# Kernel tuning notes

Measured on AMD Instinct MI355X. Metric: run time of the kernel, lower is better.

Reference implementation:

```python
import jax, jax.numpy as jnp
import numpy as np

HIDDEN = 1024
HEADS = 16
HEAD_DIM = HIDDEN // HEADS


def setup_inputs() -> dict:
    key = jax.random.key(0)
    ks = jax.random.split(key, 7)
    B, S, H = 8, 1024, HIDDEN
    hidden_states = jax.random.normal(ks[0], (B, S, H), dtype=jnp.float32)
    attention_mask = jnp.zeros((B, 1, 1, S), dtype=jnp.float32)
    # Xavier-uniform weights [out, in], zero biases (matches module init)
    limit = float(np.sqrt(6.0 / (H + H)))
    Wq = jax.random.uniform(ks[1], (H, H), minval=-limit, maxval=limit, dtype=jnp.float32)
    Wk = jax.random.uniform(ks[2], (H, H), minval=-limit, maxval=limit, dtype=jnp.float32)
    Wv = jax.random.uniform(ks[3], (H, H), minval=-limit, maxval=limit, dtype=jnp.float32)
    bq = jnp.zeros((H,), dtype=jnp.float32)
    bk = jnp.zeros((H,), dtype=jnp.float32)
    bv = jnp.zeros((H,), dtype=jnp.float32)
    return {"hidden_states": hidden_states, "attention_mask": attention_mask,
            "Wq": Wq, "bq": bq, "Wk": Wk, "bk": bk, "Wv": Wv, "bv": bv}


def _split_heads(x):
    # [B, S, H] -> [B, heads, S, head_dim]
    B, S, _ = x.shape
    return x.reshape(B, S, HEADS, HEAD_DIM).transpose(0, 2, 1, 3)


def reference(hidden_states, attention_mask, Wq, bq, Wk, bk, Wv, bv):
    # Linear projections: y = x @ W^T + b  (weights stored [out, in] as in torch)
    q = _split_heads(hidden_states @ Wq.T + bq)
    k = _split_heads(hidden_states @ Wk.T + bk)
    v = _split_heads(hidden_states @ Wv.T + bv)
    scale = 1.0 / (HEAD_DIM ** 0.5)
    scores = jnp.einsum('bhqd,bhkd->bhqk', q, k) * scale  # [B,heads,S,S]
    scores = scores + attention_mask
    probs = jax.nn.softmax(scores, axis=-1)
    # dropout is identity at inference
    ctx = jnp.einsum('bhqk,bhkd->bhqd', probs, v)
    B, _, S, _ = ctx.shape
    return ctx.transpose(0, 2, 1, 3).reshape(B, S, HIDDEN)
```

## Files before the change

### kernel.cpp

```cpp
#include <hip/hip_runtime.h>
#include <hip/hip_bf16.h>
#include <stdint.h>

#define B_ 8
#define S_ 1024
#define NH_ 16
#define D_ 64
#define H_ 1024
#define M_TOT (B_*S_)
#define LOG2E 1.44269504088896f

typedef __attribute__((ext_vector_type(8))) short short8;
typedef __attribute__((ext_vector_type(4))) float f32x4;
typedef __attribute__((ext_vector_type(16))) float f32x16;

#if __has_builtin(__builtin_amdgcn_exp2f)
#define EXP2(x) __builtin_amdgcn_exp2f(x)
#else
#define EXP2(x) __expf((x) * 0.69314718056f)
#endif

static __device__ __forceinline__ unsigned short f2bf(float f) {
  union { float f; unsigned u; } c; c.f = f;
  unsigned u = c.u;
  return (unsigned short)((u + 0x7fffu + ((u >> 16) & 1u)) >> 16);
}

static __device__ __forceinline__ void gld_lds16(void* lds, const void* g) {
  __builtin_amdgcn_global_load_lds((const __attribute__((address_space(1))) unsigned*)g,
                                   (__attribute__((address_space(3))) unsigned*)lds, 16, 0, 0);
}

#define WAIT_LGKM0() asm volatile("s_waitcnt lgkmcnt(0)" ::: "memory")
#define WAIT_VM(n)   asm volatile("s_waitcnt vmcnt(" #n ")" ::: "memory")
#define SBAR()       __builtin_amdgcn_s_barrier()
#define SCHED0()     __builtin_amdgcn_sched_barrier(0)
#define PRIO1()      __builtin_amdgcn_s_setprio(1)
#define PRIO0()      __builtin_amdgcn_s_setprio(0)

__global__ void cvt_f32_bf16(const float* __restrict__ X,
                             const float* __restrict__ Wq,
                             const float* __restrict__ Wk,
                             const float* __restrict__ Wv,
                             unsigned short* __restrict__ Xbf,
                             unsigned short* __restrict__ Wbf) {
  const long long NX = (long long)M_TOT * H_;
  const long long NW = (long long)H_ * H_;
  long long t = (long long)blockIdx.x * blockDim.x + threadIdx.x;
  const long long stride = (long long)gridDim.x * blockDim.x;
  const long long total4 = (NX + 3 * NW) >> 2;
  for (; t < total4; t += stride) {
    long long e = t << 2;
    const float* src; unsigned short* dst;
    if (e < NX) { src = X + e; dst = Xbf + e; }
    else {
      long long r = e - NX;
      int w = (int)(r / NW);
      long long o = r - (long long)w * NW;
      src = (w == 0 ? Wq : (w == 1 ? Wk : Wv)) + o;
      dst = Wbf + (long long)w * NW + o;
    }
    float4 v = *(const float4*)src;
    ushort4 u;
    u.x = f2bf(v.x); u.y = f2bf(v.y); u.z = f2bf(v.z); u.w = f2bf(v.w);
    *(ushort4*)dst = u;
  }
}

#define QBM 256
#define QBN 256
#define QBK 64
#define REG_B 32768
#define BUFSZ 65536

#define MMQ(I0, J0, AF, BF)                                               \
  _Pragma("unroll")                                                       \
  for (int a_ = 0; a_ < 4; ++a_)                                          \
    _Pragma("unroll")                                                     \
    for (int b_ = 0; b_ < 2; ++b_)                                        \
      _Pragma("unroll")                                                   \
      for (int k_ = 0; k_ < 2; ++k_)                                      \
        acc[(I0) + a_][(J0) + b_] = __builtin_amdgcn_mfma_f32_16x16x32_bf16( \
            AF[a_][k_], BF[b_][k_], acc[(I0) + a_][(J0) + b_], 0, 0, 0);

#define RD_A(BUF, MS)                                                     \
  _Pragma("unroll")                                                       \
  for (int f_ = 0; f_ < 4; ++f_)                                          \
    _Pragma("unroll")                                                     \
    for (int k_ = 0; k_ < 2; ++k_) A[f_][k_] = rdA(BUF, MS, f_, k_);

#define RD_B(DST, BUF, NS)                                                \
  _Pragma("unroll")                                                       \
  for (int f_ = 0; f_ < 2; ++f_)                                          \
    _Pragma("unroll")                                                     \
    for (int k_ = 0; k_ < 2; ++k_) DST[f_][k_] = rdB(BUF, NS, f_, k_);

__global__ __launch_bounds__(512, 1) void qkv_gemm(
    const unsigned short* __restrict__ Xbf,
    const unsigned short* __restrict__ Wbf,
    const float* __restrict__ bq, const float* __restrict__ bk,
    const float* __restrict__ bv,
    unsigned short* __restrict__ Qo, unsigned short* __restrict__ Ko,
    unsigned short* __restrict__ Vt) {
  __shared__ char lds[2 * BUFSZ];

  const int tid = threadIdx.x;
  const int w = tid >> 6;
  const int l = tid & 63;
  const int lrow = l & 15, lgrp = l >> 4;
  const int wm = w >> 2, wn = w & 3;

  const int orig = blockIdx.x;
  const int xcd = orig & 7;
  const int slot = orig >> 3;
  const int nz = slot >> 2;
  const int mtile = (xcd * 4 + (slot & 3)) * QBM;
  const int ntile = (nz & 3) * QBN;
  const int z = nz >> 2;

  const unsigned short* Wz = Wbf + (long long)z * H_ * H_;

  const int srow = l >> 3;
  const int sslot = l & 7;
  auto stageReg = [&](char* buf, int region, int half, int k0) {
    #pragma unroll
    for (int jj = 0; jj < 2; ++jj) {
      int j = w * 2 + jj;
      int row = half * 128 + j * 8 + srow;
      int so = (sslot ^ (row & 7)) * 8;
      if (region == 0)
        gld_lds16(buf + (half * 16 + j) * 1024,
                  Xbf + (long long)(mtile + row) * H_ + k0 + so);
      else
        gld_lds16(buf + REG_B + (half * 16 + j) * 1024,
                  Wz + (long long)(ntile + row) * H_ + k0 + so);
    }
  };
  auto stageOpA = [&](char* buf, int half, int k0) { stageReg(buf, (z == 2) ? 1 : 0, half, k0); };
  auto stageOpB = [&](char* buf, int half, int k0) { stageReg(buf, (z == 2) ? 0 : 1, half, k0); };

  const int offA = (z == 2) ? REG_B : 0;
  const int offB = (z == 2) ? 0 : REG_B;
  auto rdA = [&](const char* buf, int ms, int fi, int ks) -> short8 {
    int r = ms * 128 + wm * 64 + fi * 16 + lrow;
    return *(const short8*)(buf + offA + r * 128 + (((ks * 4 + lgrp) ^ (r & 7)) * 16));
  };
  auto rdB = [&](const char* buf, int ns, int fj, int ks) -> short8 {
    int r = ns * 128 + wn * 32 + fj * 16 + lrow;
    return *(const short8*)(buf + offB + r * 128 + (((ks * 4 + lgrp) ^ (r & 7)) * 16));
  };

  f32x4 acc[8][4];
  f32x4 zero = {0.f, 0.f, 0.f, 0.f};
  #pragma unroll
  for (int a = 0; a < 8; ++a)
    #pragma unroll
    for (int c = 0; c < 4; ++c) acc[a][c] = zero;

  short8 A[4][2], B0[2][2], B1[2][2];

  stageOpA(lds, 0, 0);
  stageOpB(lds, 0, 0);
  stageOpB(lds, 1, 0);
  stageOpA(lds, 1, 0);
  stageOpA(lds + BUFSZ, 0, QBK);
  SCHED0(); WAIT_VM(6); SCHED0();
  SBAR();

  #pragma unroll 1
  for (int t = 0; t < 15; ++t) {
    char* bc = lds + ((t & 1) ? BUFSZ : 0);
    char* bn = lds + ((t & 1) ? 0 : BUFSZ);
    const int k1 = (t + 1) * QBK;
    const int k2 = (t + 2) * QBK;
    const bool st2 = (t + 2 < 16);

    RD_A(bc, 0);
    RD_B(B0, bc, 0);
    stageOpB(bn, 0, k1);
    WAIT_LGKM0(); SCHED0();
    PRIO1(); MMQ(0, 0, A, B0); PRIO0();
    SCHED0(); WAIT_VM(6); SCHED0();
    SBAR();

    RD_B(B1, bc, 1);
    stageOpB(bn, 1, k1);
    WAIT_LGKM0(); SCHED0();
    PRIO1(); MMQ(0, 2, A, B1); PRIO0();
    SCHED0(); WAIT_VM(6); SCHED0();
    SBAR();

    RD_A(bc, 1);
    stageOpA(bn, 1, k1);
    WAIT_LGKM0(); SCHED0();
    PRIO1(); MMQ(4, 2, A, B1); PRIO0();
    SCHED0(); WAIT_VM(6); SCHED0();
    SBAR();

    if (st2) stageOpA(bc, 0, k2);
    PRIO1(); MMQ(4, 0, A, B0); PRIO0();
    SCHED0(); WAIT_VM(6); SCHED0();
    SBAR();
  }

  SCHED0(); WAIT_VM(0); SCHED0();
  SBAR();
  {
    char* bc = lds + BUFSZ;
    RD_A(bc, 0);
    RD_B(B0, bc, 0);
    WAIT_LGKM0(); SCHED0();
    PRIO1(); MMQ(0, 0, A, B0); PRIO0();
    RD_B(B1, bc, 1);
    WAIT_LGKM0(); SCHED0();
    PRIO1(); MMQ(0, 2, A, B1); PRIO0();
    RD_A(bc, 1);
    WAIT_LGKM0(); SCHED0();
    PRIO1(); MMQ(4, 2, A, B1); MMQ(4, 0, A, B0); PRIO0();
  }

  const float* bias = (z == 0) ? bq : (z == 1) ? bk : bv;
  if (z != 2) {
    unsigned short* O = (z == 0) ? Qo : Ko;
    #pragma unroll
    for (int nj = 0; nj < 4; ++nj) {
      int n = ntile + (nj >> 1) * 128 + wn * 32 + (nj & 1) * 16 + lrow;
      float bv_ = bias[n];
      int h = n >> 6, d = n & 63;
      #pragma unroll
      for (int mi = 0; mi < 8; ++mi)
        #pragma unroll
        for (int r = 0; r < 4; ++r) {
          int m = mtile + (mi >> 2) * 128 + wm * 64 + (mi & 3) * 16 + lgrp * 4 + r;
          float val = acc[mi][nj][r] + bv_;
          if (z == 0) val *= 0.125f * LOG2E;
          int b = m >> 10, s = m & 1023;
          O[(((long long)(b * NH_ + h)) * S_ + s) * D_ + d] = f2bf(val);
        }
    }
  } else {
    #pragma unroll
    for (int mi = 0; mi < 8; ++mi)
      #pragma unroll
      for (int r = 0; r < 4; ++r) {
        int nfull = ntile + (mi >> 2) * 128 + wm * 64 + (mi & 3) * 16 + lgrp * 4 + r;
        float bv_ = bias[nfull];
        int h = nfull >> 6, d = nfull & 63;
        #pragma unroll
        for (int nj = 0; nj < 4; ++nj) {
          int mfull = mtile + (nj >> 1) * 128 + wn * 32 + (nj & 1) * 16 + lrow;
          float val = acc[mi][nj][r] + bv_;
          int b = mfull >> 10, s = mfull & 1023;
          Vt[(((long long)(b * NH_ + h)) * D_ + d) * S_ + s] = f2bf(val);
        }
      }
  }
}

__global__ __launch_bounds__(256, 2) void attn_fused(
    const unsigned short* __restrict__ Qbf,
    const unsigned short* __restrict__ Kbf,
    const unsigned short* __restrict__ Vtb,
    const float* __restrict__ mask,
    float* __restrict__ out) {
  __shared__ char lds[2 * 16384 + 4096];
  char* ldsM = lds + 32768;
  const int tid = threadIdx.x, w = tid >> 6, l = tid & 63;
  const int l31 = l & 31, h = l >> 5;

  const int lid = blockIdx.x;
  const int xcd = lid & 7, k = lid >> 3;
  const int bh = xcd * 16 + (k >> 3);
  const int qt = k & 7;
  const int b = bh >> 4, hd = bh & 15;
  const int q0 = qt * 128 + w * 32;

  const unsigned short* Kg = Kbf + (long long)bh * S_ * D_;
  const unsigned short* Vg = Vtb + (long long)bh * D_ * S_;
  const float* mrow = mask + b * S_;

  auto stageKV = [&](int kt, char* buf) {
    const int key0 = kt * 64;
    #pragma unroll
    for (int t = 0; t < 2; ++t) {
      int j = w * 2 + t;
      int row = j * 8 + (l >> 3);
      int so = ((l & 7) ^ (row & 7)) * 8;
      gld_lds16(buf + j * 1024,        Kg + (long long)(key0 + row) * D_ + so);
      gld_lds16(buf + 8192 + j * 1024, Vg + (long long)row * S_ + key0 + so);
    }
  };

  short8 qf[4];
  #pragma unroll
  for (int ks = 0; ks < 4; ++ks)
    qf[ks] = *(const short8*)(Qbf + ((long long)bh * S_ + q0 + l31) * D_ + ks * 16 + 8 * h);
  {
    float4 mv = *(const float4*)(mrow + tid * 4);
    f32x4 mt;
    mt[0] = mv.x * LOG2E - 12.f;
    mt[1] = mv.y * LOG2E - 12.f;
    mt[2] = mv.z * LOG2E - 12.f;
    mt[3] = mv.w * LOG2E - 12.f;
    *(f32x4*)(ldsM + tid * 16) = mt;
  }
  stageKV(0, lds);
  SCHED0(); WAIT_VM(0); SCHED0();
  __syncthreads();

  f32x16 acc[2];
  #pragma unroll
  for (int db = 0; db < 2; ++db)
    #pragma unroll
    for (int r = 0; r < 16; ++r) acc[db][r] = 0.f;
  float l_run = 0.f;

  #pragma unroll 1
  for (int kt = 0; kt < S_ / 64; ++kt) {
    char* ldsK = lds + (kt & 1) * 16384;
    char* ldsV = ldsK + 8192;
    const int key0 = kt * 64;
    const bool st = (kt + 1 < S_ / 64);

    if (st) stageKV(kt + 1, lds + ((kt + 1) & 1) * 16384);

    f32x16 sc[2];
    #pragma unroll
    for (int kb = 0; kb < 2; ++kb)
      #pragma unroll
      for (int r = 0; r < 16; ++r) sc[kb][r] = 0.f;

    #pragma unroll
    for (int kb = 0; kb < 2; ++kb) {
      short8 kf[4];
      #pragma unroll
      for (int ks = 0; ks < 4; ++ks) {
        int row = kb * 32 + l31;
        int g = (2 * ks + h) ^ (row & 7);
        kf[ks] = *(const short8*)(ldsK + row * 128 + g * 16);
      }
      PRIO1();
      #pragma unroll
      for (int ks = 0; ks < 4; ++ks)
        sc[kb] = __builtin_amdgcn_mfma_f32_32x32x16_bf16(
            kf[ks], qf[ks], sc[kb], 0, 0, 0);
      PRIO0();
    }

    float sv[32];
    #pragma unroll
    for (int kb = 0; kb < 2; ++kb)
      #pragma unroll
      for (int rg = 0; rg < 4; ++rg) {
        f32x4 m4 = *(const f32x4*)(ldsM + (key0 + kb * 32 + rg * 8 + 4 * h) * 4);
        #pragma unroll
        for (int c = 0; c < 4; ++c)
          sv[kb * 16 + rg * 4 + c] = EXP2(sc[kb][rg * 4 + c] + m4[c]);
      }
    {
      float r16[16];
      #pragma unroll
      for (int i = 0; i < 16; ++i) r16[i] = sv[i] + sv[i + 16];
      #pragma unroll
      for (int i = 0; i < 8; ++i) r16[i] = r16[i] + r16[i + 8];
      #pragma unroll
      for (int i = 0; i < 4; ++i) r16[i] = r16[i] + r16[i + 4];
      float ps = (r16[0] + r16[1]) + (r16[2] + r16[3]);
      float xs = ps, ys = ps;
      asm volatile("v_permlane32_swap_b32 %0, %1" : "+v"(xs), "+v"(ys));
      l_run += xs + ys;
    }

    short8 pfrag[4];
    {
      unsigned Wd[8][2];
      #pragma unroll
      for (int j = 0; j < 8; ++j) {
        int base = (j >> 2) * 16 + (j & 3) * 4;
        asm("v_cvt_pk_bf16_f32 %0, %1, %2" : "=v"(Wd[j][0]) : "v"(sv[base + 0]), "v"(sv[base + 1]));
        asm("v_cvt_pk_bf16_f32 %0, %1, %2" : "=v"(Wd[j][1]) : "v"(sv[base + 2]), "v"(sv[base + 3]));
      }
      #pragma unroll
      for (int ks = 0; ks < 4; ++ks) {
        unsigned x0 = Wd[2 * ks][0], y0 = Wd[2 * ks + 1][0];
        unsigned x1 = Wd[2 * ks][1], y1 = Wd[2 * ks + 1][1];
        asm volatile("v_permlane32_swap_b32 %0, %1" : "+v"(x0), "+v"(y0));
        asm volatile("v_permlane32_swap_b32 %0, %1" : "+v"(x1), "+v"(y1));
        union { unsigned u[4]; short8 s; } fu;
        fu.u[0] = x0;
        fu.u[1] = x1;
        fu.u[2] = y0;
        fu.u[3] = y1;
        pfrag[ks] = fu.s;
      }
    }

    #pragma unroll
    for (int db = 0; db < 2; ++db) {
      short8 vf[4];
      #pragma unroll
      for (int ks = 0; ks < 4; ++ks) {
        int row = db * 32 + l31;
        int g = (2 * ks + h) ^ (row & 7);
        vf[ks] = *(const short8*)(ldsV + row * 128 + g * 16);
      }
      PRIO1();
      #pragma unroll
      for (int ks = 0; ks < 4; ++ks)
        acc[db] = __builtin_amdgcn_mfma_f32_32x32x16_bf16(
            vf[ks], pfrag[ks], acc[db], 0, 0, 0);
      PRIO0();
    }

    if (st) { SCHED0(); WAIT_VM(0); SCHED0(); SBAR(); }
  }

  {
    float inv = 1.0f / l_run;
    int q = q0 + l31;
    float* orow = out + ((long long)b * S_ + q) * H_ + hd * D_;
    #pragma unroll
    for (int db = 0; db < 2; ++db)
      #pragma unroll
      for (int rg = 0; rg < 4; ++rg) {
        f32x4 v4;
        #pragma unroll
        for (int c = 0; c < 4; ++c) v4[c] = acc[db][rg * 4 + c] * inv;
        *(f32x4*)(orow + db * 32 + rg * 8 + 4 * h) = v4;
      }
  }
}

extern "C" void kernel_launch(void* const* d_in, const int* in_sizes, int n_in,
                              void* d_out, int out_size, void* d_ws, size_t ws_size,
                              hipStream_t stream) {
  const float* X    = (const float*)d_in[0];
  const float* mask = (const float*)d_in[1];
  const float* Wq   = (const float*)d_in[2];
  const float* bq   = (const float*)d_in[3];
  const float* Wk   = (const float*)d_in[4];
  const float* bk   = (const float*)d_in[5];
  const float* Wv   = (const float*)d_in[6];
  const float* bv   = (const float*)d_in[7];
  float* out = (float*)d_out;

  char* ws = (char*)d_ws;
  unsigned short* Xbf = (unsigned short*)ws;
  unsigned short* Wbf = (unsigned short*)(ws + 16777216);
  unsigned short* Qb  = (unsigned short*)(ws + 23068672);
  unsigned short* Kb  = (unsigned short*)(ws + 39845888);
  unsigned short* Vt  = (unsigned short*)(ws + 56623104);

  hipLaunchKernelGGL(cvt_f32_bf16, dim3(2048), dim3(256), 0, stream,
                     X, Wq, Wk, Wv, Xbf, Wbf);
  hipLaunchKernelGGL(qkv_gemm, dim3(384), dim3(512), 0, stream,
                     Xbf, Wbf, bq, bk, bv, Qb, Kb, Vt);
  hipLaunchKernelGGL(attn_fused, dim3(1024), dim3(256), 0, stream,
                     Qb, Kb, Vt, mask, out);
}
```

Measured before the change: 119.3 us.

## Split QKV GEMM into Q/K kernel and separate V kernel with triple buffering

The fused QKV projection is split into two launches. Q/K uses the original 256x256 tiles on 256 blocks, and V gets its own kernel with 256(N)x128(M) tiles, a triple-buffered LDS pipeline and 256 blocks. The old single grid of 384 blocks gave 1.5 waves on 256 CUs, and each kernel now fills exactly one wave. The cost is an extra kernel launch, smaller V tiles with lower arithmetic intensity, and more LDS per block for the triple buffer.

Result: no change. 117.1 us, median of 2 (-1.8%).

```diff
diff --git a/kernel.cpp b/kernel.cpp
--- a/kernel.cpp
+++ b/kernel.cpp
@@ -72,6 +72,7 @@
 #define QBK 64
 #define REG_B 32768
 #define BUFSZ 65536
+#define VBUF  49152
 
 #define MMQ(I0, J0, AF, BF)                                               \
   _Pragma("unroll")                                                       \
@@ -95,13 +96,11 @@
     _Pragma("unroll")                                                     \
     for (int k_ = 0; k_ < 2; ++k_) DST[f_][k_] = rdB(BUF, NS, f_, k_);
 
-__global__ __launch_bounds__(512, 1) void qkv_gemm(
+__global__ __launch_bounds__(512, 1) void qkv_gemm_qk(
     const unsigned short* __restrict__ Xbf,
     const unsigned short* __restrict__ Wbf,
     const float* __restrict__ bq, const float* __restrict__ bk,
-    const float* __restrict__ bv,
-    unsigned short* __restrict__ Qo, unsigned short* __restrict__ Ko,
-    unsigned short* __restrict__ Vt) {
+    unsigned short* __restrict__ Qo, unsigned short* __restrict__ Ko) {
   __shared__ char lds[2 * BUFSZ];
 
   const int tid = threadIdx.x;
@@ -122,32 +121,34 @@
 
   const int srow = l >> 3;
   const int sslot = l & 7;
-  auto stageReg = [&](char* buf, int region, int half, int k0) {
+  auto stageOpA = [&](char* buf, int half, int k0) {
     #pragma unroll
     for (int jj = 0; jj < 2; ++jj) {
       int j = w * 2 + jj;
       int row = half * 128 + j * 8 + srow;
       int so = (sslot ^ (row & 7)) * 8;
-      if (region == 0)
-        gld_lds16(buf + (half * 16 + j) * 1024,
-                  Xbf + (long long)(mtile + row) * H_ + k0 + so);
-      else
-        gld_lds16(buf + REG_B + (half * 16 + j) * 1024,
-                  Wz + (long long)(ntile + row) * H_ + k0 + so);
-    }
-  };
-  auto stageOpA = [&](char* buf, int half, int k0) { stageReg(buf, (z == 2) ? 1 : 0, half, k0); };
-  auto stageOpB = [&](char* buf, int half, int k0) { stageReg(buf, (z == 2) ? 0 : 1, half, k0); };
-
-  const int offA = (z == 2) ? REG_B : 0;
-  const int offB = (z == 2) ? 0 : REG_B;
+      gld_lds16(buf + (half * 16 + j) * 1024,
+                Xbf + (long long)(mtile + row) * H_ + k0 + so);
+    }
+  };
+  auto stageOpB = [&](char* buf, int half, int k0) {
+    #pragma unroll
+    for (int jj = 0; jj < 2; ++jj) {
+      int j = w * 2 + jj;
+      int row = half * 128 + j * 8 + srow;
+      int so = (sslot ^ (row & 7)) * 8;
+      gld_lds16(buf + REG_B + (half * 16 + j) * 1024,
+                Wz + (long long)(ntile + row) * H_ + k0 + so);
+    }
+  };
+
   auto rdA = [&](const char* buf, int ms, int fi, int ks) -> short8 {
     int r = ms * 128 + wm * 64 + fi * 16 + lrow;
-    return *(const short8*)(buf + offA + r * 128 + (((ks * 4 + lgrp) ^ (r & 7)) * 16));
+    return *(const short8*)(buf + r * 128 + (((ks * 4 + lgrp) ^ (r & 7)) * 16));
   };
   auto rdB = [&](const char* buf, int ns, int fj, int ks) -> short8 {
     int r = ns * 128 + wn * 32 + fj * 16 + lrow;
-    return *(const short8*)(buf + offB + r * 128 + (((ks * 4 + lgrp) ^ (r & 7)) * 16));
+    return *(const short8*)(buf + REG_B + r * 128 + (((ks * 4 + lgrp) ^ (r & 7)) * 16));
   };
 
   f32x4 acc[8][4];
@@ -219,42 +220,134 @@
     PRIO1(); MMQ(4, 2, A, B1); MMQ(4, 0, A, B0); PRIO0();
   }
 
-  const float* bias = (z == 0) ? bq : (z == 1) ? bk : bv;
-  if (z != 2) {
-    unsigned short* O = (z == 0) ? Qo : Ko;
-    #pragma unroll
-    for (int nj = 0; nj < 4; ++nj) {
-      int n = ntile + (nj >> 1) * 128 + wn * 32 + (nj & 1) * 16 + lrow;
-      float bv_ = bias[n];
-      int h = n >> 6, d = n & 63;
-      #pragma unroll
-      for (int mi = 0; mi < 8; ++mi)
-        #pragma unroll
-        for (int r = 0; r < 4; ++r) {
-          int m = mtile + (mi >> 2) * 128 + wm * 64 + (mi & 3) * 16 + lgrp * 4 + r;
-          float val = acc[mi][nj][r] + bv_;
-          if (z == 0) val *= 0.125f * LOG2E;
-          int b = m >> 10, s = m & 1023;
-          O[(((long long)(b * NH_ + h)) * S_ + s) * D_ + d] = f2bf(val);
-        }
-    }
-  } else {
+  const float* bias = (z == 0) ? bq : bk;
+  unsigned short* O = (z == 0) ? Qo : Ko;
+  #pragma unroll
+  for (int nj = 0; nj < 4; ++nj) {
+    int n = ntile + (nj >> 1) * 128 + wn * 32 + (nj & 1) * 16 + lrow;
+    float bv_ = bias[n];
+    int h = n >> 6, d = n & 63;
     #pragma unroll
     for (int mi = 0; mi < 8; ++mi)
       #pragma unroll
       for (int r = 0; r < 4; ++r) {
-        int nfull = ntile + (mi >> 2) * 128 + wm * 64 + (mi & 3) * 16 + lgrp * 4 + r;
-        float bv_ = bias[nfull];
-        int h = nfull >> 6, d = nfull & 63;
-        #pragma unroll
-        for (int nj = 0; nj < 4; ++nj) {
-          int mfull = mtile + (nj >> 1) * 128 + wn * 32 + (nj & 1) * 16 + lrow;
-          float val = acc[mi][nj][r] + bv_;
-          int b = mfull >> 10, s = mfull & 1023;
-          Vt[(((long long)(b * NH_ + h)) * D_ + d) * S_ + s] = f2bf(val);
-        }
-      }
-  }
+        int m = mtile + (mi >> 2) * 128 + wm * 64 + (mi & 3) * 16 + lgrp * 4 + r;
+        float val = acc[mi][nj][r] + bv_;
+        if (z == 0) val *= 0.125f * LOG2E;
+        int b = m >> 10, s = m & 1023;
+        O[(((long long)(b * NH_ + h)) * S_ + s) * D_ + d] = f2bf(val);
+      }
+  }
+}
+
+__global__ __launch_bounds__(512, 1) void qkv_gemm_v(
+    const unsigned short* __restrict__ Xbf,
+    const unsigned short* __restrict__ Wbf,
+    const float* __restrict__ bv,
+    unsigned short* __restrict__ Vt) {
+  __shared__ char lds[3 * VBUF];
+
+  const int tid = threadIdx.x;
+  const int w = tid >> 6;
+  const int l = tid & 63;
+  const int lrow = l & 15, lgrp = l >> 4;
+  const int wm = w >> 2, wn = w & 3;
+
+  const int orig = blockIdx.x;
+  const int xcd = orig & 7;
+  const int slot = orig >> 3;
+  const int mtile = (xcd * 8 + (slot & 7)) * 128;
+  const int ntile = (slot >> 3) * QBN;
+
+  const unsigned short* Wz = Wbf + 2LL * H_ * H_;
+
+  const int srow = l >> 3;
+  const int sslot = l & 7;
+  auto stageW = [&](char* buf, int half, int k0) {
+    #pragma unroll
+    for (int jj = 0; jj < 2; ++jj) {
+      int j = w * 2 + jj;
+      int row = half * 128 + j * 8 + srow;
+      int so = (sslot ^ (row & 7)) * 8;
+      gld_lds16(buf + (half * 16 + j) * 1024,
+                Wz + (long long)(ntile + row) * H_ + k0 + so);
+    }
+  };
+  auto stageX = [&](char* buf, int k0) {
+    #pragma unroll
+    for (int jj = 0; jj < 2; ++jj) {
+      int j = w * 2 + jj;
+      int row = j * 8 + srow;
+      int so = (sslot ^ (row & 7)) * 8;
+      gld_lds16(buf + 32768 + j * 1024,
+                Xbf + (long long)(mtile + row) * H_ + k0 + so);
+    }
+  };
+
+  auto rdA = [&](const char* buf, int ms, int fi, int ks) -> short8 {
+    int r = ms * 128 + wm * 64 + fi * 16 + lrow;
+    return *(const short8*)(buf + r * 128 + (((ks * 4 + lgrp) ^ (r & 7)) * 16));
+  };
+  auto rdB = [&](const char* buf, int ns, int fj, int ks) -> short8 {
+    int r = wn * 32 + fj * 16 + lrow;
+    (void)ns;
+    return *(const short8*)(buf + 32768 + r * 128 + (((ks * 4 + lgrp) ^ (r & 7)) * 16));
+  };
+
+  f32x4 acc[8][2];
+  f32x4 zero = {0.f, 0.f, 0.f, 0.f};
+  #pragma unroll
+  for (int a = 0; a < 8; ++a)
+    #pragma unroll
+    for (int c = 0; c < 2; ++c) acc[a][c] = zero;
+
+  short8 A[4][2], B0[2][2];
+
+  stageW(lds, 0, 0); stageW(lds, 1, 0); stageX(lds, 0);
+  stageW(lds + VBUF, 0, QBK); stageW(lds + VBUF, 1, QBK); stageX(lds + VBUF, QBK);
+  SCHED0(); WAIT_VM(6); SCHED0();
+  SBAR();
+
+  #pragma unroll 1
+  for (int t = 0; t < 16; ++t) {
+    char* bc = lds + (t % 3) * VBUF;
+    char* b2 = lds + ((t + 2) % 3) * VBUF;
+    const int k2 = (t + 2) * QBK;
+    const bool st2 = (t + 2 < 16);
+
+    RD_A(bc, 0);
+    RD_B(B0, bc, 0);
+    if (st2) { stageW(b2, 0, k2); stageW(b2, 1, k2); }
+    WAIT_LGKM0(); SCHED0();
+    PRIO1(); MMQ(0, 0, A, B0); PRIO0();
+    SCHED0(); WAIT_VM(6); SCHED0();
+    SBAR();
+
+    RD_A(bc, 1);
+    if (st2) stageX(b2, k2);
+    WAIT_LGKM0(); SCHED0();
+    PRIO1(); MMQ(4, 0, A, B0); PRIO0();
+    SCHED0();
+    if (t < 14) { WAIT_VM(6); } else { WAIT_VM(0); }
+    SCHED0();
+    SBAR();
+  }
+
+  #pragma unroll
+  for (int mi = 0; mi < 8; ++mi)
+    #pragma unroll
+    for (int r = 0; r < 4; ++r) {
+      int nfull = ntile + (mi >> 2) * 128 + wm * 64 + (mi & 3) * 16 + lgrp * 4 + r;
+      float bv_ = bv[nfull];
+      int h = nfull >> 6, d = nfull & 63;
+      #pragma unroll
+      for (int nj = 0; nj < 2; ++nj) {
+        int mfull = mtile + wn * 32 + nj * 16 + lrow;
+        float val = acc[mi][nj][r] + bv_;
+        int b = mfull >> 10, s = mfull & 1023;
+        Vt[(((long long)(b * NH_ + h)) * D_ + d) * S_ + s] = f2bf(val);
+      }
+    }
 }
 
 __global__ __launch_bounds__(256, 2) void attn_fused(
@@ -453,8 +546,10 @@
 
   hipLaunchKernelGGL(cvt_f32_bf16, dim3(2048), dim3(256), 0, stream,
                      X, Wq, Wk, Wv, Xbf, Wbf);
-  hipLaunchKernelGGL(qkv_gemm, dim3(384), dim3(512), 0, stream,
-                     Xbf, Wbf, bq, bk, bv, Qb, Kb, Vt);
+  hipLaunchKernelGGL(qkv_gemm_qk, dim3(256), dim3(512), 0, stream,
+                     Xbf, Wbf, bq, bk, Qb, Kb);
+  hipLaunchKernelGGL(qkv_gemm_v, dim3(256), dim3(512), 0, stream,
+                     Xbf, Wbf, bv, Vt);
   hipLaunchKernelGGL(attn_fused, dim3(1024), dim3(256), 0, stream,
                      Qb, Kb, Vt, mask, out);
 }
```
